# Kernel optimization log

Hardware: AMD Instinct MI355X
Metric: run time of the kernel (lower is better)

## Reference

```python
import jax, jax.numpy as jnp
import numpy as np
import math

D_MODEL = 512
NHEAD = 8
D_FF = 2048
EPS = 1e-5


def setup_inputs() -> dict:
    key = jax.random.key(0)
    ks = jax.random.split(key, 12)
    B, S, D, F = 8, 1024, D_MODEL, D_FF
    sc_d = 1.0 / math.sqrt(D)
    sc_f = 1.0 / math.sqrt(F)
    return {
        "seq": jax.random.normal(ks[0], (B, S, D), jnp.float32),
        "Wq": jax.random.normal(ks[1], (D, D), jnp.float32) * sc_d,
        "bq": jnp.zeros((D,), jnp.float32),
        "Wk": jax.random.normal(ks[2], (D, D), jnp.float32) * sc_d,
        "bk": jnp.zeros((D,), jnp.float32),
        "Wv": jax.random.normal(ks[3], (D, D), jnp.float32) * sc_d,
        "bv": jnp.zeros((D,), jnp.float32),
        "W1": jax.random.normal(ks[4], (D, F), jnp.float32) * sc_d,
        "b1": jnp.zeros((F,), jnp.float32),
        "W2": jax.random.normal(ks[5], (F, D), jnp.float32) * sc_f,
        "b2": jnp.zeros((D,), jnp.float32),
        "gamma": jnp.ones((D,), jnp.float32),
        "beta": jnp.zeros((D,), jnp.float32),
    }


def _layernorm(x, gamma, beta):
    mu = jnp.mean(x, axis=-1, keepdims=True)
    var = jnp.mean(jnp.square(x - mu), axis=-1, keepdims=True)
    return (x - mu) * jax.lax.rsqrt(var + EPS) * gamma + beta


def reference(seq, Wq, bq, Wk, bk, Wv, bv, W1, b1, W2, b2, gamma, beta):
    B, S, D = seq.shape
    H, Dh = NHEAD, D // NHEAD
    # QKV projections, split into heads: [B, S, H, Dh]
    q = (seq @ Wq + bq).reshape(B, S, H, Dh)
    k = (seq @ Wk + bk).reshape(B, S, H, Dh)
    v = (seq @ Wv + bv).reshape(B, S, H, Dh)
    # scores [B, H, S, S]; NOTE: original applies softmax FIRST, then divides
    # by sqrt(d_model) (quirk of the source module) -- kept faithfully.
    scores = jnp.einsum('bqhd,bkhd->bhqk', q, k)
    attn = jax.nn.softmax(scores, axis=-1) / math.sqrt(D)
    attn_out = jnp.einsum('bhqk,bkhd->bqhd', attn, v).reshape(B, S, D)
    # residual + LayerNorm (dropout is identity at eval)
    out = _layernorm(seq + attn_out, gamma, beta)
    # FFN with LeakyReLU; second residual has NO layernorm in the source.
    ff = jax.nn.leaky_relu(out @ W1 + b1, negative_slope=0.01) @ W2 + b2
    return out + ff
```

## Files before the change

kernel.cpp:

```cpp
#include <hip/hip_runtime.h>

typedef __bf16 bf16;
typedef __bf16 bf16x4 __attribute__((ext_vector_type(4)));
typedef __bf16 bf16x8 __attribute__((ext_vector_type(8)));
typedef float f32x4 __attribute__((ext_vector_type(4)));
typedef float f32x16 __attribute__((ext_vector_type(16)));

#define MFMA16(a, b, c) __builtin_amdgcn_mfma_f32_16x16x32_bf16((a), (b), (c), 0, 0, 0)
#define MFMA32(a, b, c) __builtin_amdgcn_mfma_f32_32x32x16_bf16((a), (b), (c), 0, 0, 0)
#define PLSWAP(a, b) asm("v_permlane32_swap_b32 %0, %1" : "+v"(a), "+v"(b))

typedef const void __attribute__((address_space(1)))* gas1;
typedef void __attribute__((address_space(3)))* las3;
#define ASYNC16(g, l) __builtin_amdgcn_global_load_lds((gas1)(g), (las3)(l), 16, 0, 0)

__device__ __forceinline__ unsigned pk2(float lo, float hi) {
  unsigned short a = __builtin_bit_cast(unsigned short, (bf16)lo);
  unsigned short b = __builtin_bit_cast(unsigned short, (bf16)hi);
  return (unsigned)a | ((unsigned)b << 16);
}

__global__ __launch_bounds__(256) void cvt_f32_bf16(const float* __restrict__ in,
                                                    bf16* __restrict__ out, int n8) {
  int i = blockIdx.x * 256 + threadIdx.x;
  if (i < n8) {
    float4 a = ((const float4*)in)[2 * i];
    float4 b = ((const float4*)in)[2 * i + 1];
    bf16x8 v;
    v[0] = (bf16)a.x; v[1] = (bf16)a.y; v[2] = (bf16)a.z; v[3] = (bf16)a.w;
    v[4] = (bf16)b.x; v[5] = (bf16)b.y; v[6] = (bf16)b.z; v[7] = (bf16)b.w;
    ((bf16x8*)out)[i] = v;
  }
}

__global__ __launch_bounds__(256) void transpose_cvt(const float* __restrict__ in,
                                                     bf16* __restrict__ out, int K, int N) {
  __shared__ float tile[32][33];
  int tx = threadIdx.x, ty = threadIdx.y;
  int n0 = blockIdx.x * 32, k0 = blockIdx.y * 32;
#pragma unroll
  for (int i = 0; i < 4; i++) tile[ty + i * 8][tx] = in[(long)(k0 + ty + i * 8) * N + n0 + tx];
  __syncthreads();
#pragma unroll
  for (int i = 0; i < 4; i++)
    out[(long)(n0 + ty + i * 8) * K + k0 + tx] = (bf16)tile[tx][ty + i * 8];
}

__global__ __launch_bounds__(256) void transpose_cvt_qkv(const float* __restrict__ Wq,
                                                         const float* __restrict__ Wk,
                                                         const float* __restrict__ Wv,
                                                         bf16* __restrict__ out) {
  __shared__ float tile[32][33];
  int tx = threadIdx.x, ty = threadIdx.y;
  int which = blockIdx.z;
  const float* in = which == 0 ? Wq : (which == 1 ? Wk : Wv);
  bf16* o = out + (long)which * 512 * 512;
  int n0 = blockIdx.x * 32, k0 = blockIdx.y * 32;
#pragma unroll
  for (int i = 0; i < 4; i++) tile[ty + i * 8][tx] = in[(long)(k0 + ty + i * 8) * 512 + n0 + tx];
  __syncthreads();
#pragma unroll
  for (int i = 0; i < 4; i++)
    o[(long)(n0 + ty + i * 8) * 512 + k0 + tx] = (bf16)tile[tx][ty + i * 8];
}

__global__ __launch_bounds__(256) void concat_bias(const float* __restrict__ bq,
                                                   const float* __restrict__ bk,
                                                   const float* __restrict__ bv,
                                                   float* __restrict__ outb) {
  int i = blockIdx.x * 256 + threadIdx.x;
  if (i < 512) outb[i] = bq[i];
  else if (i < 1024) outb[i] = bk[i - 512];
  else if (i < 1536) outb[i] = bv[i - 1024];
}

template <int ACT, int RESID, int VSPLIT, typename OutT>
__global__ __launch_bounds__(256, 2)
void gemm_bt(const bf16* __restrict__ A, const bf16* __restrict__ BT,
             const float* __restrict__ bias, const bf16* __restrict__ resid,
             OutT* __restrict__ C, bf16* __restrict__ vt,
             int K, int lda, int ldb, int ldc) {
  __shared__ __align__(16) char As[128 * 128];
  __shared__ __align__(16) char Bs[128 * 128];
  const int tid = threadIdx.x;
  const int l = tid & 63, w = tid >> 6;
  const int lrow = l & 15, lhi = l >> 4;
  const int wr = w >> 1, wc = w & 1;
  const long brow = (long)blockIdx.y * 128;
  const long bcol = (long)blockIdx.x * 128;

  f32x4 zero = {0.f, 0.f, 0.f, 0.f};
  f32x4 acc[4][4];
#pragma unroll
  for (int m = 0; m < 4; m++)
#pragma unroll
    for (int n = 0; n < 4; n++) acc[m][n] = zero;

  for (int kt = 0; kt < K; kt += 64) {
    __syncthreads();
#pragma unroll
    for (int c = 0; c < 4; c++) {
      int idx = c * 256 + tid;
      int row = idx >> 3;
      int cole = ((idx & 7) ^ (row & 7)) * 8;
      ASYNC16(A + (brow + row) * lda + kt + cole, As + idx * 16);
      ASYNC16(BT + (bcol + row) * ldb + kt + cole, Bs + idx * 16);
    }
    __syncthreads();
    bf16x8 af[4][2], bfr[4][2];
#pragma unroll
    for (int m = 0; m < 4; m++) {
      int row = wr * 64 + m * 16 + lrow;
      int base = row * 128 + lhi * 16;
      int sw = (row & 7) << 4;
      af[m][0] = *(const bf16x8*)(As + (base ^ sw));
      af[m][1] = *(const bf16x8*)(As + ((base + 64) ^ sw));
    }
#pragma unroll
    for (int n = 0; n < 4; n++) {
      int row = wc * 64 + n * 16 + lrow;
      int base = row * 128 + lhi * 16;
      int sw = (row & 7) << 4;
      bfr[n][0] = *(const bf16x8*)(Bs + (base ^ sw));
      bfr[n][1] = *(const bf16x8*)(Bs + ((base + 64) ^ sw));
    }
#pragma unroll
    for (int m = 0; m < 4; m++)
#pragma unroll
      for (int n = 0; n < 4; n++) {
        acc[m][n] = MFMA16(af[m][0], bfr[n][0], acc[m][n]);
        acc[m][n] = MFMA16(af[m][1], bfr[n][1], acc[m][n]);
      }
  }

  if (VSPLIT && bcol >= 1024) {
#pragma unroll
    for (int m = 0; m < 4; m++) {
#pragma unroll
      for (int n = 0; n < 4; n++) {
        long col = bcol + wc * 64 + n * 16 + lrow;
        float bv = bias[col];
        int cc = (int)col - 1024;
        int hh = cc >> 6, dd = cc & 63;
        long row0 = brow + wr * 64 + m * 16 + lhi * 4;
        int b = (int)(row0 >> 10), s0 = (int)(row0 & 1023);
        bf16x4 v4;
#pragma unroll
        for (int r = 0; r < 4; r++) v4[r] = (bf16)(acc[m][n][r] + bv);
        *(bf16x4*)(vt + ((long)(b * 8 + hh) * 64 + dd) * 1024 + s0) = v4;
      }
    }
    return;
  }

#pragma unroll
  for (int m = 0; m < 4; m++) {
#pragma unroll
    for (int n = 0; n < 4; n++) {
      long col = bcol + wc * 64 + n * 16 + lrow;
      float bv = bias[col];
#pragma unroll
      for (int r = 0; r < 4; r++) {
        long row = brow + wr * 64 + m * 16 + lhi * 4 + r;
        float v = acc[m][n][r] + bv;
        if (ACT) v = v > 0.f ? v : 0.01f * v;
        if (RESID) v += (float)resid[row * ldc + col];
        C[row * ldc + col] = (OutT)v;
      }
    }
  }
}

__global__ __launch_bounds__(256, 2)
void attn_fwd(const bf16* __restrict__ QKV, const bf16* __restrict__ Vtg,
              bf16* __restrict__ attn_out) {
  __shared__ __align__(16) char Ks[2][64 * 128];
  __shared__ __align__(16) char Vs[2][64 * 128];
  const int tid = threadIdx.x;
  const int l = tid & 63, w = tid >> 6;
  const int q = l & 31, hi = l >> 5;
  const int h = blockIdx.y;
  const long rowbase = (long)blockIdx.z * 1024;
  const int q0 = blockIdx.x * 128;
  const float LOG2E = 1.4426950408889634f;

  const bf16* Kb = QKV + 512;
  const bf16* Vb = Vtg + ((long)blockIdx.z * 8 + h) * 64 * 1024;

  auto stage = [&](int buf, int kt) {
#pragma unroll
    for (int c = 0; c < 2; c++) {
      int idx = c * 256 + tid;
      int row = idx >> 3;
      int cole = ((idx & 7) ^ (row & 7)) * 8;
      ASYNC16(Kb + (rowbase + kt * 64 + row) * 1536 + h * 64 + cole, Ks[buf] + idx * 16);
      ASYNC16(Vb + row * 1024 + kt * 64 + cole, Vs[buf] + idx * 16);
    }
  };

  bf16x8 aq[4];
  {
    long qrow = rowbase + q0 + w * 32 + q;
    const bf16* p = QKV + qrow * 1536 + h * 64 + hi * 8;
    aq[0] = *(const bf16x8*)(p);
    aq[1] = *(const bf16x8*)(p + 16);
    aq[2] = *(const bf16x8*)(p + 32);
    aq[3] = *(const bf16x8*)(p + 48);
  }
  asm volatile("" ::"v"(aq[0]), "v"(aq[1]), "v"(aq[2]), "v"(aq[3]));

  f32x16 o0, o1;
#pragma unroll
  for (int i = 0; i < 16; i++) { o0[i] = 0.f; o1[i] = 0.f; }
  float m_run = -1e30f, l_run = 0.f;

  stage(0, 0);
  int cur = 0;

  for (int kt = 0; kt < 16; ++kt) {
    asm volatile("" ::: "memory");
    __builtin_amdgcn_s_barrier();
    asm volatile("" ::: "memory");
    stage(cur ^ 1, (kt + 1) & 15);
    asm volatile("s_waitcnt vmcnt(4)" ::: "memory");
    __builtin_amdgcn_sched_barrier(0);
    __builtin_amdgcn_s_barrier();
    asm volatile("" ::: "memory");

    const char* Kc = Ks[cur];
    const char* Vc = Vs[cur];

    f32x16 s0, s1;
#pragma unroll
    for (int i = 0; i < 16; i++) { s0[i] = 0.f; s1[i] = 0.f; }
    __builtin_amdgcn_s_setprio(1);
#pragma unroll
    for (int t = 0; t < 2; t++) {
      f32x16 c;
#pragma unroll
      for (int i = 0; i < 16; i++) c[i] = 0.f;
      int row = t * 32 + q;
      int sw = (row & 7) << 4;
#pragma unroll
      for (int sd = 0; sd < 4; sd++) {
        bf16x8 kf = *(const bf16x8*)(Kc + ((row * 128 + sd * 32 + hi * 16) ^ sw));
        c = MFMA32(kf, aq[sd], c);
      }
      if (t) s1 = c; else s0 = c;
    }
    __builtin_amdgcn_s_setprio(0);

    float tmax = s0[0];
#pragma unroll
    for (int i = 1; i < 16; i++) tmax = fmaxf(tmax, s0[i]);
#pragma unroll
    for (int i = 0; i < 16; i++) tmax = fmaxf(tmax, s1[i]);
    tmax = fmaxf(tmax, __shfl_xor(tmax, 32));
    float mn = fmaxf(m_run, tmax);
    float al = __builtin_exp2f((m_run - mn) * LOG2E);
    float mh = mn * LOG2E;
    m_run = mn;
    float p0[16], p1[16];
    float ps = 0.f;
#pragma unroll
    for (int i = 0; i < 16; i++) {
      p0[i] = __builtin_exp2f(__builtin_fmaf(s0[i], LOG2E, -mh));
      ps += p0[i];
    }
#pragma unroll
    for (int i = 0; i < 16; i++) {
      p1[i] = __builtin_exp2f(__builtin_fmaf(s1[i], LOG2E, -mh));
      ps += p1[i];
    }
    ps += __shfl_xor(ps, 32);
    l_run = l_run * al + ps;
#pragma unroll
    for (int i = 0; i < 16; i++) { o0[i] *= al; o1[i] *= al; }

    bf16x8 pa[4];
    {
      unsigned a0 = pk2(p0[0], p0[1]), b0 = pk2(p0[4], p0[5]);
      unsigned a1 = pk2(p0[2], p0[3]), b1 = pk2(p0[6], p0[7]);
      unsigned a2 = pk2(p0[8], p0[9]), b2 = pk2(p0[12], p0[13]);
      unsigned a3 = pk2(p0[10], p0[11]), b3 = pk2(p0[14], p0[15]);
      PLSWAP(a0, b0); PLSWAP(a1, b1); PLSWAP(a2, b2); PLSWAP(a3, b3);
      uint4 w0 = {a0, a1, b0, b1};
      uint4 w1 = {a2, a3, b2, b3};
      pa[0] = __builtin_bit_cast(bf16x8, w0);
      pa[1] = __builtin_bit_cast(bf16x8, w1);
      unsigned c0 = pk2(p1[0], p1[1]), d0 = pk2(p1[4], p1[5]);
      unsigned c1 = pk2(p1[2], p1[3]), d1 = pk2(p1[6], p1[7]);
      unsigned c2 = pk2(p1[8], p1[9]), d2 = pk2(p1[12], p1[13]);
      unsigned c3 = pk2(p1[10], p1[11]), d3 = pk2(p1[14], p1[15]);
      PLSWAP(c0, d0); PLSWAP(c1, d1); PLSWAP(c2, d2); PLSWAP(c3, d3);
      uint4 w2 = {c0, c1, d0, d1};
      uint4 w3 = {c2, c3, d2, d3};
      pa[2] = __builtin_bit_cast(bf16x8, w2);
      pa[3] = __builtin_bit_cast(bf16x8, w3);
    }

    __builtin_amdgcn_s_setprio(1);
    {
      int row = q;
      int sw = (row & 7) << 4;
#pragma unroll
      for (int ks = 0; ks < 4; ks++) {
        bf16x8 vf = *(const bf16x8*)(Vc + ((row * 128 + ks * 32 + hi * 16) ^ sw));
        o0 = MFMA32(vf, pa[ks], o0);
      }
      row = 32 + q;
      sw = (row & 7) << 4;
#pragma unroll
      for (int ks = 0; ks < 4; ks++) {
        bf16x8 vf = *(const bf16x8*)(Vc + ((row * 128 + ks * 32 + hi * 16) ^ sw));
        o1 = MFMA32(vf, pa[ks], o1);
      }
    }
    __builtin_amdgcn_s_setprio(0);
    cur ^= 1;
  }

  float fac = 0.044194173824159216f / l_run;
  long qrow = rowbase + q0 + w * 32 + q;
  bf16* op = attn_out + qrow * 512 + h * 64;
#pragma unroll
  for (int t = 0; t < 4; t++) {
    bf16x4 v0, v1;
#pragma unroll
    for (int u = 0; u < 4; u++) {
      v0[u] = (bf16)(o0[4 * t + u] * fac);
      v1[u] = (bf16)(o1[4 * t + u] * fac);
    }
    *(bf16x4*)(op + 8 * t + 4 * hi) = v0;
    *(bf16x4*)(op + 32 + 8 * t + 4 * hi) = v1;
  }
}

__global__ __launch_bounds__(256) void ln_kernel(const float* __restrict__ seq,
                                                 const bf16* __restrict__ attn,
                                                 const float* __restrict__ gamma,
                                                 const float* __restrict__ beta,
                                                 bf16* __restrict__ out) {
  int row = blockIdx.x;
  int tid = threadIdx.x;
  long base = (long)row * 512;
  float x0 = seq[base + tid] + (float)attn[base + tid];
  float x1 = seq[base + 256 + tid] + (float)attn[base + 256 + tid];
  float s = x0 + x1, ss = x0 * x0 + x1 * x1;
#pragma unroll
  for (int mm = 1; mm < 64; mm <<= 1) {
    s += __shfl_xor(s, mm);
    ss += __shfl_xor(ss, mm);
  }
  __shared__ float red[8];
  int w = tid >> 6, l = tid & 63;
  if (l == 0) { red[w] = s; red[4 + w] = ss; }
  __syncthreads();
  s = red[0] + red[1] + red[2] + red[3];
  ss = red[4] + red[5] + red[6] + red[7];
  float mu = s * (1.f / 512.f);
  float var = ss * (1.f / 512.f) - mu * mu;
  float rs = rsqrtf(var + 1e-5f);
  out[base + tid] = (bf16)((x0 - mu) * rs * gamma[tid] + beta[tid]);
  out[base + 256 + tid] = (bf16)((x1 - mu) * rs * gamma[tid + 256] + beta[tid + 256]);
}

extern "C" void kernel_launch(void* const* d_in, const int* in_sizes, int n_in,
                              void* d_out, int out_size, void* d_ws, size_t ws_size,
                              hipStream_t stream) {
  const float* seq = (const float*)d_in[0];
  const float* Wq = (const float*)d_in[1];
  const float* bq = (const float*)d_in[2];
  const float* Wk = (const float*)d_in[3];
  const float* bk = (const float*)d_in[4];
  const float* Wv = (const float*)d_in[5];
  const float* bv = (const float*)d_in[6];
  const float* W1 = (const float*)d_in[7];
  const float* b1 = (const float*)d_in[8];
  const float* W2 = (const float*)d_in[9];
  const float* b2 = (const float*)d_in[10];
  const float* gamma = (const float*)d_in[11];
  const float* beta = (const float*)d_in[12];
  float* out = (float*)d_out;

  char* ws = (char*)d_ws;
  if (ws_size < 89659392u) return;
  bf16* seq_bf = (bf16*)(ws + 0);
  bf16* qkvT = (bf16*)(ws + 8388608);
  bf16* W1T = (bf16*)(ws + 9961472);
  bf16* W2T = (bf16*)(ws + 12058624);
  float* bqkv = (float*)(ws + 14155776);
  bf16* QKV = (bf16*)(ws + 14161920);
  bf16* attn = (bf16*)(ws + 39327744);
  bf16* ln = (bf16*)(ws + 47716352);
  bf16* hidden = (bf16*)(ws + 56104960);
  bf16* vt = (bf16*)(ws + 56104960);

  cvt_f32_bf16<<<2048, 256, 0, stream>>>(seq, seq_bf, 524288);
  transpose_cvt_qkv<<<dim3(16, 16, 3), dim3(32, 8), 0, stream>>>(Wq, Wk, Wv, qkvT);
  transpose_cvt<<<dim3(64, 16), dim3(32, 8), 0, stream>>>(W1, W1T, 512, 2048);
  transpose_cvt<<<dim3(16, 64), dim3(32, 8), 0, stream>>>(W2, W2T, 2048, 512);
  concat_bias<<<6, 256, 0, stream>>>(bq, bk, bv, bqkv);

  gemm_bt<0, 0, 1, bf16><<<dim3(12, 64), 256, 0, stream>>>(
      seq_bf, qkvT, bqkv, (const bf16*)nullptr, QKV, vt, 512, 512, 512, 1536);
  attn_fwd<<<dim3(8, 8, 8), 256, 0, stream>>>(QKV, vt, attn);
  ln_kernel<<<8192, 256, 0, stream>>>(seq, attn, gamma, beta, ln);
  gemm_bt<1, 0, 0, bf16><<<dim3(16, 64), 256, 0, stream>>>(
      ln, W1T, b1, (const bf16*)nullptr, hidden, (bf16*)nullptr, 512, 512, 512, 2048);
  gemm_bt<0, 1, 0, float><<<dim3(4, 64), 256, 0, stream>>>(
      hidden, W2T, b2, ln, out, (bf16*)nullptr, 2048, 2048, 2048, 512);
}
```

Measured before the change: 152.9 us.

## Load attention K/V fragments directly from global memory, drop LDS staging

New measurement: 187.3 us. +22.5%, slower.

```diff
diff --git a/kernel.cpp b/kernel.cpp
--- a/kernel.cpp
+++ b/kernel.cpp
@@ -171,32 +171,22 @@
   }
 }
 
-__global__ __launch_bounds__(256, 2)
+__global__ __launch_bounds__(128, 4)
 void attn_fwd(const bf16* __restrict__ QKV, const bf16* __restrict__ Vtg,
               bf16* __restrict__ attn_out) {
-  __shared__ __align__(16) char Ks[2][64 * 128];
-  __shared__ __align__(16) char Vs[2][64 * 128];
+  const int bid = blockIdx.x;
+  const int bh = bid & 63;
+  const int qt = bid >> 6;
+  const int b = bh >> 3, h = bh & 7;
   const int tid = threadIdx.x;
   const int l = tid & 63, w = tid >> 6;
   const int q = l & 31, hi = l >> 5;
-  const int h = blockIdx.y;
-  const long rowbase = (long)blockIdx.z * 1024;
-  const int q0 = blockIdx.x * 128;
+  const long rowbase = (long)b * 1024;
+  const int q0 = qt * 64;
   const float LOG2E = 1.4426950408889634f;
 
-  const bf16* Kb = QKV + 512;
-  const bf16* Vb = Vtg + ((long)blockIdx.z * 8 + h) * 64 * 1024;
-
-  auto stage = [&](int buf, int kt) {
-#pragma unroll
-    for (int c = 0; c < 2; c++) {
-      int idx = c * 256 + tid;
-      int row = idx >> 3;
-      int cole = ((idx & 7) ^ (row & 7)) * 8;
-      ASYNC16(Kb + (rowbase + kt * 64 + row) * 1536 + h * 64 + cole, Ks[buf] + idx * 16);
-      ASYNC16(Vb + row * 1024 + kt * 64 + cole, Vs[buf] + idx * 16);
-    }
-  };
+  const bf16* kb = QKV + 512 + rowbase * 1536 + h * 64 + hi * 8;
+  const bf16* vb = Vtg + (long)bh * 64 * 1024 + hi * 8;
 
   bf16x8 aq[4];
   {
@@ -214,41 +204,38 @@
   for (int i = 0; i < 16; i++) { o0[i] = 0.f; o1[i] = 0.f; }
   float m_run = -1e30f, l_run = 0.f;
 
-  stage(0, 0);
-  int cur = 0;
-
   for (int kt = 0; kt < 16; ++kt) {
-    asm volatile("" ::: "memory");
-    __builtin_amdgcn_s_barrier();
-    asm volatile("" ::: "memory");
-    stage(cur ^ 1, (kt + 1) & 15);
-    asm volatile("s_waitcnt vmcnt(4)" ::: "memory");
-    __builtin_amdgcn_sched_barrier(0);
-    __builtin_amdgcn_s_barrier();
-    asm volatile("" ::: "memory");
-
-    const char* Kc = Ks[cur];
-    const char* Vc = Vs[cur];
+    bf16x8 kf0[4], kf1[4];
+    {
+      const bf16* k0p = kb + (long)(kt * 64 + q) * 1536;
+      const bf16* k1p = kb + (long)(kt * 64 + 32 + q) * 1536;
+#pragma unroll
+      for (int sd = 0; sd < 4; sd++) {
+        kf0[sd] = *(const bf16x8*)(k0p + sd * 16);
+        kf1[sd] = *(const bf16x8*)(k1p + sd * 16);
+      }
+    }
 
     f32x16 s0, s1;
 #pragma unroll
     for (int i = 0; i < 16; i++) { s0[i] = 0.f; s1[i] = 0.f; }
     __builtin_amdgcn_s_setprio(1);
 #pragma unroll
-    for (int t = 0; t < 2; t++) {
-      f32x16 c;
-#pragma unroll
-      for (int i = 0; i < 16; i++) c[i] = 0.f;
-      int row = t * 32 + q;
-      int sw = (row & 7) << 4;
-#pragma unroll
-      for (int sd = 0; sd < 4; sd++) {
-        bf16x8 kf = *(const bf16x8*)(Kc + ((row * 128 + sd * 32 + hi * 16) ^ sw));
-        c = MFMA32(kf, aq[sd], c);
-      }
-      if (t) s1 = c; else s0 = c;
-    }
+    for (int sd = 0; sd < 4; sd++) s0 = MFMA32(kf0[sd], aq[sd], s0);
+#pragma unroll
+    for (int sd = 0; sd < 4; sd++) s1 = MFMA32(kf1[sd], aq[sd], s1);
     __builtin_amdgcn_s_setprio(0);
+
+    bf16x8 vf0[4], vf1[4];
+    {
+      const bf16* v0p = vb + (long)q * 1024 + kt * 64;
+      const bf16* v1p = vb + (long)(32 + q) * 1024 + kt * 64;
+#pragma unroll
+      for (int ks = 0; ks < 4; ks++) {
+        vf0[ks] = *(const bf16x8*)(v0p + ks * 16);
+        vf1[ks] = *(const bf16x8*)(v1p + ks * 16);
+      }
+    }
 
     float tmax = s0[0];
 #pragma unroll
@@ -300,24 +287,11 @@
     }
 
     __builtin_amdgcn_s_setprio(1);
-    {
-      int row = q;
-      int sw = (row & 7) << 4;
-#pragma unroll
-      for (int ks = 0; ks < 4; ks++) {
-        bf16x8 vf = *(const bf16x8*)(Vc + ((row * 128 + ks * 32 + hi * 16) ^ sw));
-        o0 = MFMA32(vf, pa[ks], o0);
-      }
-      row = 32 + q;
-      sw = (row & 7) << 4;
-#pragma unroll
-      for (int ks = 0; ks < 4; ks++) {
-        bf16x8 vf = *(const bf16x8*)(Vc + ((row * 128 + ks * 32 + hi * 16) ^ sw));
-        o1 = MFMA32(vf, pa[ks], o1);
-      }
-    }
+#pragma unroll
+    for (int ks = 0; ks < 4; ks++) o0 = MFMA32(vf0[ks], pa[ks], o0);
+#pragma unroll
+    for (int ks = 0; ks < 4; ks++) o1 = MFMA32(vf1[ks], pa[ks], o1);
     __builtin_amdgcn_s_setprio(0);
-    cur ^= 1;
   }
 
   float fac = 0.044194173824159216f / l_run;
@@ -404,7 +378,7 @@
 
   gemm_bt<0, 0, 1, bf16><<<dim3(12, 64), 256, 0, stream>>>(
       seq_bf, qkvT, bqkv, (const bf16*)nullptr, QKV, vt, 512, 512, 512, 1536);
-  attn_fwd<<<dim3(8, 8, 8), 256, 0, stream>>>(QKV, vt, attn);
+  attn_fwd<<<1024, 128, 0, stream>>>(QKV, vt, attn);
   ln_kernel<<<8192, 256, 0, stream>>>(seq, attn, gamma, beta, ln);
   gemm_bt<1, 0, 0, bf16><<<dim3(16, 64), 256, 0, stream>>>(
       ln, W1T, b1, (const bf16*)nullptr, hidden, (bf16*)nullptr, 512, 512, 512, 2048);
```
